# Kernel optimization log

Measured on AMD Instinct MI355X. Metric: run time of the kernel, lower is better.

Reference implementation:

```python
import jax, jax.numpy as jnp
import numpy as np

VOCAB, E, H, HOPS, HEADS = 32000, 128, 256, 3, 4
N, TM, WLEN, TQ = 32, 50, 20, 20


def _gru(x_tbe, h0, Wih, Whh, bih, bhh):
    # x_tbe: [T, B, E] time-major; h0: [B, H]. PyTorch GRU gate order (r, z, n).
    def step(h, xt):
        gi = xt @ Wih.T + bih
        gh = h @ Whh.T + bhh
        ir, iz, inn = jnp.split(gi, 3, axis=-1)
        hr, hz, hn = jnp.split(gh, 3, axis=-1)
        r = jax.nn.sigmoid(ir + hr)
        z = jax.nn.sigmoid(iz + hz)
        n = jnp.tanh(inn + r * hn)
        return (1.0 - z) * n + z * h, None
    h, _ = jax.lax.scan(step, h0, x_tbe)
    return h


def setup_inputs() -> dict:
    key = jax.random.key(0)
    ks = jax.random.split(key, 24)
    f32 = jnp.float32
    emb = jax.random.uniform(ks[0], (VOCAB, E), f32, -3 ** 0.5, 3 ** 0.5)
    emb = emb.at[0].set(0.0)  # padding_idx=0
    s = 0.05
    inp = {
        'stories': jax.random.randint(ks[1], (N, TM, WLEN), 0, VOCAB),
        'questions': jax.random.randint(ks[2], (N, TQ), 0, VOCAB),
        'emb': emb,
        'q_Wih': jax.random.normal(ks[3], (3 * H, E), f32) * s,
        'q_Whh': jax.random.normal(ks[4], (3 * H, H), f32) * s,
        'q_bih': jnp.zeros((3 * H,), f32),
        'q_bhh': jnp.zeros((3 * H,), f32),
        'i_Wih': jax.random.normal(ks[5], (3 * H, E), f32) * s,
        'i_Whh': jax.random.normal(ks[6], (3 * H, H), f32) * s,
        'i_bih': jnp.zeros((3 * H,), f32),
        'i_bhh': jnp.zeros((3 * H,), f32),
        'Wm': jax.random.normal(ks[7], (HOPS, HEADS, H, H), f32) * s,
        'Wo_w': jax.random.normal(ks[8], (HOPS, H, HEADS * H), f32) * s,
        'Wo_b': jnp.full((HOPS, H), 0.01, f32),
        'ft_W1': jax.random.normal(ks[9], (H, H), f32) * s,
        'ft_b1': jnp.full((H,), 0.01, f32),
        'ft_W2': jax.random.normal(ks[10], (H, H), f32) * s,
        'ft_b2': jnp.full((H,), 0.01, f32),
        'g_W1': jax.random.normal(ks[11], (3 * H, 3 * H), f32) * s,
        'g_b1': jnp.full((3 * H,), 0.01, f32),
        'g_W2': jax.random.normal(ks[12], (3 * H, 3 * H), f32) * s,
        'g_b2': jnp.full((3 * H,), 0.01, f32),
        'V_w': jax.random.normal(ks[13], (VOCAB, 3 * H), f32) * s,
    }
    return inp


def reference(stories, questions, emb, q_Wih, q_Whh, q_bih, q_bhh,
              i_Wih, i_Whh, i_bih, i_bhh, Wm, Wo_w, Wo_b,
              ft_W1, ft_b1, ft_W2, ft_b2, g_W1, g_b1, g_W2, g_b2, V_w):
    n, tm, _ = stories.shape
    h = i_Whh.shape[1]
    hops, heads = Wm.shape[0], Wm.shape[1]

    # ---- input module: per-batch-item GRU; hidden state carries across batch items (as in source loop) ----
    story_embs = emb[stories]  # [N, TM, W, E]
    def bstep(hid, se):  # se: [TM, W, E]
        hid2 = _gru(jnp.swapaxes(se, 0, 1), hid, i_Wih, i_Whh, i_bih, i_bhh)
        return hid2, hid2
    _, memory = jax.lax.scan(bstep, jnp.zeros((tm, h), emb.dtype), story_embs)  # [N, TM, H]

    # ---- question module ----
    q_emb = emb[questions]  # [N, TQ, E]
    q = _gru(jnp.swapaxes(q_emb, 0, 1), jnp.zeros((n, h), emb.dtype), q_Wih, q_Whh, q_bih, q_bhh)  # [N, H]

    def ft(x):
        return jax.nn.relu(jax.nn.relu(x @ ft_W1.T + ft_b1) @ ft_W2.T + ft_b2)

    # ---- multi-hop attention controllers ----
    o_k = ft(q)
    buffers = []
    for hp in range(hops):
        proj = jnp.tanh(jnp.einsum('ntd,hed->nhte', memory, Wm[hp]))      # [N,heads,TM,H]
        scores = jax.nn.softmax(jnp.einsum('nhte,ne->nht', proj, o_k), axis=-1)
        rep = jnp.einsum('nht,ntd->nhd', scores, memory)                   # [N,heads,H]
        buf = rep.reshape(n, heads * h) @ Wo_w[hp].T + Wo_b[hp]            # [N,H]
        buffers.append(buf)
        o_k = ft(buf)
    wb = jnp.stack(buffers, axis=1)  # [N, HOPS, H]

    # ---- RM: all-pairs relation MLP (dropout = identity in eval) ----
    npair = hops * hops
    left = jnp.broadcast_to(wb[:, None, :, :], (n, hops, hops, h)).reshape(n, npair, h)
    right = jnp.broadcast_to(wb[:, :, None, :], (n, hops, hops, h)).reshape(n, npair, h)
    qx = jnp.broadcast_to(q[:, None, :], (n, npair, h))
    comb = jnp.concatenate([left, right, qx], axis=-1)                     # [N, HOPS^2, 3H]
    g = jax.nn.relu(jax.nn.relu(comb @ g_W1.T + g_b1) @ g_W2.T + g_b2)
    reasoning = g.sum(axis=1)                                              # [N, 3H]
    return reasoning @ V_w.T                                               # [N, VOCAB]
```

## Files before the change

kernel.cpp:

```cpp
#include <hip/hip_runtime.h>
#include <cmath>

#define VOCABN 32000
#define EE 128
#define HH 256
#define H3 768
#define HOPSN 3
#define HEADSN 4
#define NB 32
#define TMN 50
#define WLENN 20
#define TQN 20
#define NPOS (NB*TMN*WLENN)
#define NQPOS (NB*TQN)

#define OFF_MEM    0
#define OFF_Q      (OFF_MEM + NB*TMN*HH)
#define OFF_OK     (OFF_Q + NB*HH)
#define OFF_WB     (OFF_OK + NB*HH)
#define OFF_REP    (OFF_WB + NB*HOPSN*HH)
#define OFF_REAS   (OFF_REP + NB*HEADSN*HH)
#define OFF_Y1     (OFF_REAS + NB*H3)
#define OFF_PROJ   (OFF_Y1 + NB*9*H3)
#define OFF_GI     (OFF_PROJ + NB*12*TMN*HH)

typedef __fp16 h2 __attribute__((ext_vector_type(2)));

__device__ __forceinline__ float sigm(float x) { return 1.f / (1.f + expf(-x)); }

__device__ __forceinline__ unsigned packh2(float x, float y) {
    h2 h = __builtin_amdgcn_cvt_pkrtz(x, y);
    return __builtin_bit_cast(unsigned, h);
}

__device__ __forceinline__ float fdot2u(unsigned a, unsigned b, float c) {
    return __builtin_amdgcn_fdot2(__builtin_bit_cast(h2, a),
                                  __builtin_bit_cast(h2, b), c, false);
}

#define LW(v, base, i8) { const float4 A_ = reinterpret_cast<const float4*>(base)[2*(i8)];     \
                          const float4 B_ = reinterpret_cast<const float4*>(base)[2*(i8)+1];   \
                          v.x = packh2(A_.x, A_.y); v.y = packh2(A_.z, A_.w);                  \
                          v.z = packh2(B_.x, B_.y); v.w = packh2(B_.z, B_.w); }

#define GIB 64
__global__ __launch_bounds__(768) void k_gi(const int* __restrict__ stories,
                                            const int* __restrict__ questions,
                                            const float* __restrict__ emb,
                                            const float* __restrict__ iWih,
                                            const float* __restrict__ qWih,
                                            const float* __restrict__ ibih, const float* __restrict__ ibhh,
                                            const float* __restrict__ qbih, const float* __restrict__ qbhh,
                                            float* __restrict__ ws)
{
    __shared__ unsigned xs[GIB][EE / 2];
    __fp16* __restrict__ gi = (__fp16*)(ws + OFF_GI);
    const int j = threadIdx.x;
    const bool isq = blockIdx.x >= (NPOS / GIB);
    const int pblk = isq ? (blockIdx.x - NPOS / GIB) : blockIdx.x;
    const int p0 = pblk * GIB;
    const size_t g0 = (isq ? (size_t)NPOS : 0) + (size_t)p0;
    const int* __restrict__ toks = isq ? (questions + p0) : (stories + p0);
    const float* __restrict__ Wih = isq ? qWih : iWih;
    const float* __restrict__ bih = isq ? qbih : ibih;
    const float* __restrict__ bhh = isq ? qbhh : ibhh;
    const float bias = (j < 2 * HH) ? (bih[j] + bhh[j]) : bih[j];
    const float* wrowp = Wih + (size_t)j * EE;
    uint4 v_0, v_1, v_2, v_3, v_4, v_5, v_6, v_7, v_8, v_9, v_10, v_11, v_12, v_13, v_14, v_15;
    LW(v_0, wrowp, 0)  LW(v_1, wrowp, 1)  LW(v_2, wrowp, 2)  LW(v_3, wrowp, 3)
    LW(v_4, wrowp, 4)  LW(v_5, wrowp, 5)  LW(v_6, wrowp, 6)  LW(v_7, wrowp, 7)
    LW(v_8, wrowp, 8)  LW(v_9, wrowp, 9)  LW(v_10, wrowp, 10) LW(v_11, wrowp, 11)
    LW(v_12, wrowp, 12) LW(v_13, wrowp, 13) LW(v_14, wrowp, 14) LW(v_15, wrowp, 15)

    for (int idx = j; idx < GIB * (EE / 2); idx += H3) {
        const int p = idx >> 6, c = idx & 63;
        const int tok = toks[p];
        const float2 e2 = reinterpret_cast<const float2*>(emb + (size_t)tok * EE)[c];
        xs[p][c] = packh2(e2.x, e2.y);
    }
    __syncthreads();

#define DOTG(i) { const uint4 xv = x4[i];                                     \
    acc = fdot2u(xv.x, v_##i.x, acc); acc = fdot2u(xv.y, v_##i.y, acc);       \
    acc = fdot2u(xv.z, v_##i.z, acc); acc = fdot2u(xv.w, v_##i.w, acc); }

    for (int p = 0; p < GIB; ++p) {
        const uint4* x4 = reinterpret_cast<const uint4*>(&xs[p][0]);
        float acc = bias;
        DOTG(0)  DOTG(1)  DOTG(2)  DOTG(3)  DOTG(4)  DOTG(5)  DOTG(6)  DOTG(7)
        DOTG(8)  DOTG(9)  DOTG(10) DOTG(11) DOTG(12) DOTG(13) DOTG(14) DOTG(15)
        gi[(g0 + p) * H3 + j] = (__fp16)acc;
    }
#undef DOTG
}

#define LDSF 22016
__global__ __attribute__((amdgpu_flat_work_group_size(512, 512), amdgpu_waves_per_eu(2, 2)))
void k_gru8(
    const float* __restrict__ iWhh, const float* __restrict__ qWhh,
    const float* __restrict__ ibhh, const float* __restrict__ qbhh,
    float* __restrict__ ws)
{
    __shared__ float ldsb[LDSF];
    unsigned* hp32 = (unsigned*)ldsb;
    float* red = ldsb + 128;
    const int tid = threadIdx.x;
    const int j = tid & 255, kh = tid >> 8;
    const int blk = blockIdx.x;
    const bool isq = blk >= TMN;
    const float* __restrict__ Whh = isq ? qWhh : iWhh;
    const float* row0 = Whh + (size_t)j * HH + kh * 128;
    const float* row1 = Whh + (size_t)(HH + j) * HH + kh * 128;
    const float* row2 = Whh + (size_t)(2 * HH + j) * HH + kh * 128;
    uint4 w0_0, w0_1, w0_2, w0_3, w0_4, w0_5, w0_6, w0_7,
          w0_8, w0_9, w0_10, w0_11, w0_12, w0_13, w0_14, w0_15;
    uint4 w1_0, w1_1, w1_2, w1_3, w1_4, w1_5, w1_6, w1_7,
          w1_8, w1_9, w1_10, w1_11, w1_12, w1_13, w1_14, w1_15;
    uint4 w2_0, w2_1, w2_2, w2_3, w2_4, w2_5, w2_6, w2_7,
          w2_8, w2_9, w2_10, w2_11, w2_12, w2_13, w2_14, w2_15;
    LW(w0_0, row0, 0)  LW(w0_1, row0, 1)  LW(w0_2, row0, 2)  LW(w0_3, row0, 3)
    LW(w0_4, row0, 4)  LW(w0_5, row0, 5)  LW(w0_6, row0, 6)  LW(w0_7, row0, 7)
    LW(w0_8, row0, 8)  LW(w0_9, row0, 9)  LW(w0_10, row0, 10) LW(w0_11, row0, 11)
    LW(w0_12, row0, 12) LW(w0_13, row0, 13) LW(w0_14, row0, 14) LW(w0_15, row0, 15)
    LW(w1_0, row1, 0)  LW(w1_1, row1, 1)  LW(w1_2, row1, 2)  LW(w1_3, row1, 3)
    LW(w1_4, row1, 4)  LW(w1_5, row1, 5)  LW(w1_6, row1, 6)  LW(w1_7, row1, 7)
    LW(w1_8, row1, 8)  LW(w1_9, row1, 9)  LW(w1_10, row1, 10) LW(w1_11, row1, 11)
    LW(w1_12, row1, 12) LW(w1_13, row1, 13) LW(w1_14, row1, 14) LW(w1_15, row1, 15)
    LW(w2_0, row2, 0)  LW(w2_1, row2, 1)  LW(w2_2, row2, 2)  LW(w2_3, row2, 3)
    LW(w2_4, row2, 4)  LW(w2_5, row2, 5)  LW(w2_6, row2, 6)  LW(w2_7, row2, 7)
    LW(w2_8, row2, 8)  LW(w2_9, row2, 9)  LW(w2_10, row2, 10) LW(w2_11, row2, 11)
    LW(w2_12, row2, 12) LW(w2_13, row2, 13) LW(w2_14, row2, 14) LW(w2_15, row2, 15)

    float bnH = 0.f, hstate = 0.f;
    if (kh == 0) bnH = (isq ? qbhh : ibhh)[2 * HH + j];
    if (tid < HH / 2) hp32[tid] = 0u;
    const __fp16* __restrict__ gib = (const __fp16*)(ws + OFF_GI)
                                     + (isq ? (size_t)NPOS * H3 : 0);
    float* __restrict__ memv = ws + OFF_MEM;
    float* __restrict__ qv   = ws + OFF_Q;
    __syncthreads();

#define DOT(i) { const uint4 hv = hp4[kh * 16 + (i)];                        \
    a0 = fdot2u(hv.x, w0_##i.x, a0); a0 = fdot2u(hv.y, w0_##i.y, a0);        \
    a0 = fdot2u(hv.z, w0_##i.z, a0); a0 = fdot2u(hv.w, w0_##i.w, a0);        \
    a1 = fdot2u(hv.x, w1_##i.x, a1); a1 = fdot2u(hv.y, w1_##i.y, a1);        \
    a1 = fdot2u(hv.z, w1_##i.z, a1); a1 = fdot2u(hv.w, w1_##i.w, a1);        \
    a2 = fdot2u(hv.x, w2_##i.x, a2); a2 = fdot2u(hv.y, w2_##i.y, a2);        \
    a2 = fdot2u(hv.z, w2_##i.z, a2); a2 = fdot2u(hv.w, w2_##i.w, a2); }

    const int nOuter = isq ? 1 : NB;
    const int c = isq ? (blk - TMN) : blk;
    for (int n = 0; n < nOuter; ++n) {
        for (int t = 0; t < WLENN; ++t) {
            const int pos = isq ? (c * TQN + t) : ((n * TMN + c) * WLENN + t);
            float gir = 0.f, giz = 0.f, gin = 0.f;
            if (kh == 0) {
                const size_t gb = (size_t)pos * H3;
                gir = (float)gib[gb + j];
                giz = (float)gib[gb + HH + j];
                gin = (float)gib[gb + 2 * HH + j];
            }
            float a0 = 0.f, a1 = 0.f, a2 = 0.f;
            const uint4* hp4 = reinterpret_cast<const uint4*>(hp32);
            DOT(0)  DOT(1)  DOT(2)  DOT(3)  DOT(4)  DOT(5)  DOT(6)  DOT(7)
            DOT(8)  DOT(9)  DOT(10) DOT(11) DOT(12) DOT(13) DOT(14) DOT(15)
            if (kh == 1) { red[j * 5 + 0] = a0; red[j * 5 + 1] = a1; red[j * 5 + 2] = a2; }
            __syncthreads();
            if (kh == 0) {
                const float* rr = red + j * 5;
                const float r  = sigm(a0 + rr[0] + gir);
                const float z  = sigm(a1 + rr[1] + giz);
                const float nn = tanhf(gin + r * (a2 + rr[2] + bnH));
                hstate = (1.f - z) * nn + z * hstate;
                reinterpret_cast<__fp16*>(hp32)[j] = (__fp16)hstate;
                if (t == WLENN - 1) {
                    if (isq) qv[c * HH + j] = hstate;
                    else     memv[(size_t)(n * TMN + c) * HH + j] = hstate;
                }
            }
            __syncthreads();
        }
    }
#undef DOT
}

__global__ __launch_bounds__(256) void k_ft(const float* __restrict__ src, float* __restrict__ dst,
                                            const float* __restrict__ W1, const float* __restrict__ b1,
                                            const float* __restrict__ W2, const float* __restrict__ b2)
{
    __shared__ float xr[HH];
    __shared__ float y1[HH];
    const int n = blockIdx.x, j = threadIdx.x;
    xr[j] = src[n * HH + j];
    __syncthreads();
    float acc = b1[j];
    const float4* w1 = reinterpret_cast<const float4*>(W1 + j * HH);
    #pragma unroll 4
    for (int k4 = 0; k4 < HH / 4; ++k4) {
        const float4 w = w1[k4];
        const float4 x = *reinterpret_cast<const float4*>(&xr[k4 * 4]);
        acc = fmaf(x.x, w.x, fmaf(x.y, w.y, fmaf(x.z, w.z, fmaf(x.w, w.w, acc))));
    }
    y1[j] = fmaxf(acc, 0.f);
    __syncthreads();
    acc = b2[j];
    const float4* w2 = reinterpret_cast<const float4*>(W2 + j * HH);
    #pragma unroll 4
    for (int k4 = 0; k4 < HH / 4; ++k4) {
        const float4 w = w2[k4];
        const float4 x = *reinterpret_cast<const float4*>(&y1[k4 * 4]);
        acc = fmaf(x.x, w.x, fmaf(x.y, w.y, fmaf(x.z, w.z, fmaf(x.w, w.w, acc))));
    }
    dst[n * HH + j] = fmaxf(acc, 0.f);
}

__global__ __launch_bounds__(256) void k_proj(const float* __restrict__ Wm, float* __restrict__ ws)
{
    __shared__ float mem_s[TMN][HH];
    const int n = blockIdx.x / 12, he = blockIdx.x % 12;
    const int e = threadIdx.x;
    const float* __restrict__ memory = ws + OFF_MEM + n * TMN * HH;
    for (int idx = e; idx < TMN * HH; idx += HH)
        (&mem_s[0][0])[idx] = memory[idx];
    __syncthreads();
    float p[TMN];
    #pragma unroll
    for (int t = 0; t < TMN; ++t) p[t] = 0.f;
    const float4* wrow = reinterpret_cast<const float4*>(Wm + ((size_t)he * HH + e) * HH);
    for (int d4 = 0; d4 < HH / 4; ++d4) {
        const float4 w = wrow[d4];
        #pragma unroll
        for (int t = 0; t < TMN; ++t) {
            const float4 m = *reinterpret_cast<const float4*>(&mem_s[t][d4 * 4]);
            p[t] = fmaf(m.x, w.x, fmaf(m.y, w.y, fmaf(m.z, w.z, fmaf(m.w, w.w, p[t]))));
        }
    }
    float* __restrict__ proj = ws + OFF_PROJ + ((size_t)(n * 12 + he) * TMN) * HH;
    #pragma unroll
    for (int t = 0; t < TMN; ++t) proj[t * HH + e] = tanhf(p[t]);
}

__global__ __launch_bounds__(256) void k_attn2(float* __restrict__ ws, int hp)
{
    __shared__ float wred[4][TMN];
    __shared__ float sc[TMN];
    const int n = blockIdx.x / HEADSN, hh = blockIdx.x % HEADSN;
    const int e = threadIdx.x;
    const float* __restrict__ proj = ws + OFF_PROJ + ((size_t)(n * 12 + hp * HEADSN + hh) * TMN) * HH;
    const float* __restrict__ memory = ws + OFF_MEM + n * TMN * HH;
    const float okv = (ws + OFF_OK)[n * HH + e];
    const int lane = e & 63, wv = e >> 6;
    #pragma unroll 10
    for (int t = 0; t < TMN; ++t) {
        float v = proj[t * HH + e] * okv;
        #pragma unroll
        for (int off = 32; off > 0; off >>= 1) v += __shfl_xor(v, off);
        if (lane == 0) wred[wv][t] = v;
    }
    __syncthreads();
    if (e < TMN) sc[e] = wred[0][e] + wred[1][e] + wred[2][e] + wred[3][e];
    __syncthreads();
    if (e == 0) {
        float mx = sc[0];
        for (int t = 1; t < TMN; ++t) mx = fmaxf(mx, sc[t]);
        float sum = 0.f;
        for (int t = 0; t < TMN; ++t) { const float ex = expf(sc[t] - mx); sc[t] = ex; sum += ex; }
        const float inv = 1.f / sum;
        for (int t = 0; t < TMN; ++t) sc[t] *= inv;
    }
    __syncthreads();
    float r = 0.f;
    #pragma unroll 10
    for (int t = 0; t < TMN; ++t) r = fmaf(sc[t], memory[t * HH + e], r);
    (ws + OFF_REP)[(n * HEADSN + hh) * HH + e] = r;
}

__global__ __launch_bounds__(256) void k_buf(const float* __restrict__ Wo_w, const float* __restrict__ Wo_b,
                                             const float* __restrict__ W1, const float* __restrict__ b1,
                                             const float* __restrict__ W2, const float* __restrict__ b2,
                                             float* __restrict__ ws, int hp)
{
    __shared__ float repf[HEADSN * HH];
    __shared__ float bufs[HH];
    __shared__ float y1[HH];
    const int n = blockIdx.x, j = threadIdx.x;
    const float* __restrict__ rep = ws + OFF_REP + n * HEADSN * HH;
    for (int idx = j; idx < HEADSN * HH; idx += HH) repf[idx] = rep[idx];
    __syncthreads();
    float acc = Wo_b[hp * HH + j];
    const float4* wrow = reinterpret_cast<const float4*>(Wo_w + ((size_t)hp * HH + j) * (HEADSN * HH));
    #pragma unroll 4
    for (int c4 = 0; c4 < HEADSN * HH / 4; ++c4) {
        const float4 w = wrow[c4];
        const float4 x = *reinterpret_cast<const float4*>(&repf[c4 * 4]);
        acc = fmaf(x.x, w.x, fmaf(x.y, w.y, fmaf(x.z, w.z, fmaf(x.w, w.w, acc))));
    }
    (ws + OFF_WB)[(n * HOPSN + hp) * HH + j] = acc;
    bufs[j] = acc;
    __syncthreads();
    float a1 = b1[j];
    const float4* w1 = reinterpret_cast<const float4*>(W1 + j * HH);
    #pragma unroll 4
    for (int k4 = 0; k4 < HH / 4; ++k4) {
        const float4 w = w1[k4];
        const float4 x = *reinterpret_cast<const float4*>(&bufs[k4 * 4]);
        a1 = fmaf(x.x, w.x, fmaf(x.y, w.y, fmaf(x.z, w.z, fmaf(x.w, w.w, a1))));
    }
    y1[j] = fmaxf(a1, 0.f);
    __syncthreads();
    float a2 = b2[j];
    const float4* w2 = reinterpret_cast<const float4*>(W2 + j * HH);
    #pragma unroll 4
    for (int k4 = 0; k4 < HH / 4; ++k4) {
        const float4 w = w2[k4];
        const float4 x = *reinterpret_cast<const float4*>(&y1[k4 * 4]);
        a2 = fmaf(x.x, w.x, fmaf(x.y, w.y, fmaf(x.z, w.z, fmaf(x.w, w.w, a2))));
    }
    (ws + OFF_OK)[n * HH + j] = fmaxf(a2, 0.f);
}

__global__ __launch_bounds__(256) void k_rm1(const float* __restrict__ gW1, const float* __restrict__ gb1,
                                             float* __restrict__ ws)
{
    __shared__ float comb[9 * H3];
    const int n = blockIdx.x / 3, ot = blockIdx.x % 3;
    const int o = ot * 256 + threadIdx.x;
    const float* __restrict__ wb = ws + OFF_WB + n * HOPSN * HH;
    const float* __restrict__ qv = ws + OFF_Q + n * HH;
    for (int idx = threadIdx.x; idx < 9 * H3; idx += 256) {
        const int p = idx / H3, cc = idx - p * H3;
        const int ii = p / 3, jj = p % 3;
        float v;
        if (cc < HH)           v = wb[jj * HH + cc];
        else if (cc < 2 * HH)  v = wb[ii * HH + (cc - HH)];
        else                   v = qv[cc - 2 * HH];
        comb[idx] = v;
    }
    __syncthreads();
    float acc[9];
    const float b = gb1[o];
    #pragma unroll
    for (int p = 0; p < 9; ++p) acc[p] = b;
    const float4* w1 = reinterpret_cast<const float4*>(gW1 + (size_t)o * H3);
    for (int c4 = 0; c4 < H3 / 4; ++c4) {
        const float4 w = w1[c4];
        #pragma unroll
        for (int p = 0; p < 9; ++p) {
            const float4 x = *reinterpret_cast<const float4*>(&comb[p * H3 + c4 * 4]);
            acc[p] = fmaf(x.x, w.x, fmaf(x.y, w.y, fmaf(x.z, w.z, fmaf(x.w, w.w, acc[p]))));
        }
    }
    float* __restrict__ y1 = ws + OFF_Y1 + (size_t)n * 9 * H3;
    #pragma unroll
    for (int p = 0; p < 9; ++p) y1[p * H3 + o] = fmaxf(acc[p], 0.f);
}

__global__ __launch_bounds__(256) void k_rm2(const float* __restrict__ gW2, const float* __restrict__ gb2,
                                             float* __restrict__ ws)
{
    __shared__ float y1s[9 * H3];
    const int n = blockIdx.x / 3, ot = blockIdx.x % 3;
    const int o = ot * 256 + threadIdx.x;
    const float* __restrict__ y1 = ws + OFF_Y1 + (size_t)n * 9 * H3;
    for (int idx = threadIdx.x; idx < 9 * H3; idx += 256) y1s[idx] = y1[idx];
    __syncthreads();
    float acc[9];
    const float b = gb2[o];
    #pragma unroll
    for (int p = 0; p < 9; ++p) acc[p] = b;
    const float4* w2 = reinterpret_cast<const float4*>(gW2 + (size_t)o * H3);
    for (int c4 = 0; c4 < H3 / 4; ++c4) {
        const float4 w = w2[c4];
        #pragma unroll
        for (int p = 0; p < 9; ++p) {
            const float4 x = *reinterpret_cast<const float4*>(&y1s[p * H3 + c4 * 4]);
            acc[p] = fmaf(x.x, w.x, fmaf(x.y, w.y, fmaf(x.z, w.z, fmaf(x.w, w.w, acc[p]))));
        }
    }
    float s = 0.f;
    #pragma unroll
    for (int p = 0; p < 9; ++p) s += fmaxf(acc[p], 0.f);
    (ws + OFF_REAS)[n * H3 + o] = s;
}

#define RST 36
__global__ __launch_bounds__(256) void k_out(const float* __restrict__ V_w, const float* __restrict__ ws,
                                             float* __restrict__ out)
{
    __shared__ float rsT[H3 * RST];
    const int tid = threadIdx.x;
    const int v = blockIdx.x * 128 + (tid & 127);
    const int nh = tid >> 7;
    for (int idx = tid; idx < NB * H3; idx += 256) {
        const int n = idx / H3, d = idx - n * H3;
        rsT[d * RST + n] = (ws + OFF_REAS)[idx];
    }
    __syncthreads();
    float acc[16];
    #pragma unroll
    for (int i = 0; i < 16; ++i) acc[i] = 0.f;
    const float4* vw = reinterpret_cast<const float4*>(V_w + (size_t)v * H3);
    for (int d4 = 0; d4 < H3 / 4; ++d4) {
        const float4 w = vw[d4];
        #pragma unroll
        for (int dd = 0; dd < 4; ++dd) {
            const float wd = (dd == 0) ? w.x : (dd == 1) ? w.y : (dd == 2) ? w.z : w.w;
            const float* rr = &rsT[(d4 * 4 + dd) * RST + nh * 16];
            #pragma unroll
            for (int q = 0; q < 4; ++q) {
                const float4 r4 = *reinterpret_cast<const float4*>(rr + 4 * q);
                acc[4 * q + 0] = fmaf(wd, r4.x, acc[4 * q + 0]);
                acc[4 * q + 1] = fmaf(wd, r4.y, acc[4 * q + 1]);
                acc[4 * q + 2] = fmaf(wd, r4.z, acc[4 * q + 2]);
                acc[4 * q + 3] = fmaf(wd, r4.w, acc[4 * q + 3]);
            }
        }
    }
    #pragma unroll
    for (int i = 0; i < 16; ++i)
        out[(size_t)(nh * 16 + i) * VOCABN + v] = acc[i];
}

extern "C" void kernel_launch(void* const* d_in, const int* in_sizes, int n_in,
                              void* d_out, int out_size, void* d_ws, size_t ws_size,
                              hipStream_t stream)
{
    const int*   stories   = (const int*)d_in[0];
    const int*   questions = (const int*)d_in[1];
    const float* emb   = (const float*)d_in[2];
    const float* qWih  = (const float*)d_in[3];
    const float* qWhh  = (const float*)d_in[4];
    const float* qbih  = (const float*)d_in[5];
    const float* qbhh  = (const float*)d_in[6];
    const float* iWih  = (const float*)d_in[7];
    const float* iWhh  = (const float*)d_in[8];
    const float* ibih  = (const float*)d_in[9];
    const float* ibhh  = (const float*)d_in[10];
    const float* Wm    = (const float*)d_in[11];
    const float* Wo_w  = (const float*)d_in[12];
    const float* Wo_b  = (const float*)d_in[13];
    const float* ftW1  = (const float*)d_in[14];
    const float* ftb1  = (const float*)d_in[15];
    const float* ftW2  = (const float*)d_in[16];
    const float* ftb2  = (const float*)d_in[17];
    const float* gW1   = (const float*)d_in[18];
    const float* gb1   = (const float*)d_in[19];
    const float* gW2   = (const float*)d_in[20];
    const float* gb2   = (const float*)d_in[21];
    const float* V_w   = (const float*)d_in[22];
    float* ws  = (float*)d_ws;
    float* out = (float*)d_out;

    hipLaunchKernelGGL(k_gi, dim3((NPOS + NQPOS) / GIB), dim3(H3), 0, stream,
                       stories, questions, emb, iWih, qWih, ibih, ibhh, qbih, qbhh, ws);
    hipLaunchKernelGGL(k_gru8, dim3(TMN + NB), dim3(512), 0, stream,
                       iWhh, qWhh, ibhh, qbhh, ws);
    hipLaunchKernelGGL(k_ft, dim3(NB), dim3(HH), 0, stream, ws + OFF_Q, ws + OFF_OK, ftW1, ftb1, ftW2, ftb2);
    hipLaunchKernelGGL(k_proj, dim3(NB * 12), dim3(256), 0, stream, Wm, ws);
    for (int hp = 0; hp < HOPSN; ++hp) {
        hipLaunchKernelGGL(k_attn2, dim3(NB * HEADSN), dim3(256), 0, stream, ws, hp);
        hipLaunchKernelGGL(k_buf, dim3(NB), dim3(256), 0, stream, Wo_w, Wo_b, ftW1, ftb1, ftW2, ftb2, ws, hp);
    }
    hipLaunchKernelGGL(k_rm1, dim3(NB * 3), dim3(256), 0, stream, gW1, gb1, ws);
    hipLaunchKernelGGL(k_rm2, dim3(NB * 3), dim3(256), 0, stream, gW2, gb2, ws);
    hipLaunchKernelGGL(k_out, dim3(VOCABN / 128), dim3(256), 0, stream, V_w, ws, out);
}
```

Measured before the change: 1.361 ms.

## Fuse feature transform, hop attention, buffer and relation MLP into one tail kernel

Replaces the separate k_ft, per-hop k_attn2/k_buf launches and k_rm1/k_rm2 with one k_tail kernel: one 1024-thread block per batch item keeps memory, o_k, rep and the relation-MLP intermediates in LDS. The goal is to remove about nine kernel launches and the global round-trips of intermediate buffers between them. In exchange, the relation-MLP stage now runs on 32 blocks instead of 96, and each block streams the full g_W1 and g_W2 matrices. The GRU kernel also drops its oversized padded LDS allocation in favour of small exact arrays, which may change how its blocks are placed on CUs.

```diff
diff --git a/kernel.cpp b/kernel.cpp
--- a/kernel.cpp
+++ b/kernel.cpp
@@ -94,16 +94,14 @@
 #undef DOTG
 }
 
-#define LDSF 22016
 __global__ __attribute__((amdgpu_flat_work_group_size(512, 512), amdgpu_waves_per_eu(2, 2)))
-void k_gru8(
+void k_gru7(
     const float* __restrict__ iWhh, const float* __restrict__ qWhh,
     const float* __restrict__ ibhh, const float* __restrict__ qbhh,
     float* __restrict__ ws)
 {
-    __shared__ float ldsb[LDSF];
-    unsigned* hp32 = (unsigned*)ldsb;
-    float* red = ldsb + 128;
+    __shared__ unsigned hp32[HH / 2];
+    __shared__ float red[HH * 5];
     const int tid = threadIdx.x;
     const int j = tid & 255, kh = tid >> 8;
     const int blk = blockIdx.x;
@@ -184,36 +182,6 @@
 #undef DOT
 }
 
-__global__ __launch_bounds__(256) void k_ft(const float* __restrict__ src, float* __restrict__ dst,
-                                            const float* __restrict__ W1, const float* __restrict__ b1,
-                                            const float* __restrict__ W2, const float* __restrict__ b2)
-{
-    __shared__ float xr[HH];
-    __shared__ float y1[HH];
-    const int n = blockIdx.x, j = threadIdx.x;
-    xr[j] = src[n * HH + j];
-    __syncthreads();
-    float acc = b1[j];
-    const float4* w1 = reinterpret_cast<const float4*>(W1 + j * HH);
-    #pragma unroll 4
-    for (int k4 = 0; k4 < HH / 4; ++k4) {
-        const float4 w = w1[k4];
-        const float4 x = *reinterpret_cast<const float4*>(&xr[k4 * 4]);
-        acc = fmaf(x.x, w.x, fmaf(x.y, w.y, fmaf(x.z, w.z, fmaf(x.w, w.w, acc))));
-    }
-    y1[j] = fmaxf(acc, 0.f);
-    __syncthreads();
-    acc = b2[j];
-    const float4* w2 = reinterpret_cast<const float4*>(W2 + j * HH);
-    #pragma unroll 4
-    for (int k4 = 0; k4 < HH / 4; ++k4) {
-        const float4 w = w2[k4];
-        const float4 x = *reinterpret_cast<const float4*>(&y1[k4 * 4]);
-        acc = fmaf(x.x, w.x, fmaf(x.y, w.y, fmaf(x.z, w.z, fmaf(x.w, w.w, acc))));
-    }
-    dst[n * HH + j] = fmaxf(acc, 0.f);
-}
-
 __global__ __launch_bounds__(256) void k_proj(const float* __restrict__ Wm, float* __restrict__ ws)
 {
     __shared__ float mem_s[TMN][HH];
@@ -240,94 +208,115 @@
     for (int t = 0; t < TMN; ++t) proj[t * HH + e] = tanhf(p[t]);
 }
 
-__global__ __launch_bounds__(256) void k_attn2(float* __restrict__ ws, int hp)
-{
-    __shared__ float wred[4][TMN];
-    __shared__ float sc[TMN];
-    const int n = blockIdx.x / HEADSN, hh = blockIdx.x % HEADSN;
-    const int e = threadIdx.x;
-    const float* __restrict__ proj = ws + OFF_PROJ + ((size_t)(n * 12 + hp * HEADSN + hh) * TMN) * HH;
-    const float* __restrict__ memory = ws + OFF_MEM + n * TMN * HH;
-    const float okv = (ws + OFF_OK)[n * HH + e];
-    const int lane = e & 63, wv = e >> 6;
-    #pragma unroll 10
-    for (int t = 0; t < TMN; ++t) {
-        float v = proj[t * HH + e] * okv;
-        #pragma unroll
-        for (int off = 32; off > 0; off >>= 1) v += __shfl_xor(v, off);
-        if (lane == 0) wred[wv][t] = v;
-    }
-    __syncthreads();
-    if (e < TMN) sc[e] = wred[0][e] + wred[1][e] + wred[2][e] + wred[3][e];
-    __syncthreads();
-    if (e == 0) {
-        float mx = sc[0];
-        for (int t = 1; t < TMN; ++t) mx = fmaxf(mx, sc[t]);
-        float sum = 0.f;
-        for (int t = 0; t < TMN; ++t) { const float ex = expf(sc[t] - mx); sc[t] = ex; sum += ex; }
-        const float inv = 1.f / sum;
-        for (int t = 0; t < TMN; ++t) sc[t] *= inv;
-    }
-    __syncthreads();
-    float r = 0.f;
-    #pragma unroll 10
-    for (int t = 0; t < TMN; ++t) r = fmaf(sc[t], memory[t * HH + e], r);
-    (ws + OFF_REP)[(n * HEADSN + hh) * HH + e] = r;
-}
-
-__global__ __launch_bounds__(256) void k_buf(const float* __restrict__ Wo_w, const float* __restrict__ Wo_b,
-                                             const float* __restrict__ W1, const float* __restrict__ b1,
-                                             const float* __restrict__ W2, const float* __restrict__ b2,
-                                             float* __restrict__ ws, int hp)
-{
+__global__ __launch_bounds__(1024) void k_tail(
+    const float* __restrict__ Wo_w, const float* __restrict__ Wo_b,
+    const float* __restrict__ ftW1, const float* __restrict__ ftb1,
+    const float* __restrict__ ftW2, const float* __restrict__ ftb2,
+    const float* __restrict__ gW1, const float* __restrict__ gb1,
+    const float* __restrict__ gW2, const float* __restrict__ gb2,
+    float* __restrict__ ws)
+{
+    __shared__ float mem_s[TMN][HH];
+    __shared__ float ok_s[HH];
+    __shared__ float xr[HH];
+    __shared__ float yft[HH];
+    __shared__ float red4[4][HH];
+    __shared__ float wred[4][4][TMN];
+    __shared__ float sc4[4][TMN];
     __shared__ float repf[HEADSN * HH];
     __shared__ float bufs[HH];
-    __shared__ float y1[HH];
-    const int n = blockIdx.x, j = threadIdx.x;
-    const float* __restrict__ rep = ws + OFF_REP + n * HEADSN * HH;
-    for (int idx = j; idx < HEADSN * HH; idx += HH) repf[idx] = rep[idx];
-    __syncthreads();
-    float acc = Wo_b[hp * HH + j];
-    const float4* wrow = reinterpret_cast<const float4*>(Wo_w + ((size_t)hp * HH + j) * (HEADSN * HH));
-    #pragma unroll 4
-    for (int c4 = 0; c4 < HEADSN * HH / 4; ++c4) {
-        const float4 w = wrow[c4];
-        const float4 x = *reinterpret_cast<const float4*>(&repf[c4 * 4]);
-        acc = fmaf(x.x, w.x, fmaf(x.y, w.y, fmaf(x.z, w.z, fmaf(x.w, w.w, acc))));
-    }
-    (ws + OFF_WB)[(n * HOPSN + hp) * HH + j] = acc;
-    bufs[j] = acc;
-    __syncthreads();
-    float a1 = b1[j];
-    const float4* w1 = reinterpret_cast<const float4*>(W1 + j * HH);
-    #pragma unroll 4
-    for (int k4 = 0; k4 < HH / 4; ++k4) {
-        const float4 w = w1[k4];
-        const float4 x = *reinterpret_cast<const float4*>(&bufs[k4 * 4]);
-        a1 = fmaf(x.x, w.x, fmaf(x.y, w.y, fmaf(x.z, w.z, fmaf(x.w, w.w, a1))));
-    }
-    y1[j] = fmaxf(a1, 0.f);
-    __syncthreads();
-    float a2 = b2[j];
-    const float4* w2 = reinterpret_cast<const float4*>(W2 + j * HH);
-    #pragma unroll 4
-    for (int k4 = 0; k4 < HH / 4; ++k4) {
-        const float4 w = w2[k4];
-        const float4 x = *reinterpret_cast<const float4*>(&y1[k4 * 4]);
-        a2 = fmaf(x.x, w.x, fmaf(x.y, w.y, fmaf(x.z, w.z, fmaf(x.w, w.w, a2))));
-    }
-    (ws + OFF_OK)[n * HH + j] = fmaxf(a2, 0.f);
-}
-
-__global__ __launch_bounds__(256) void k_rm1(const float* __restrict__ gW1, const float* __restrict__ gb1,
-                                             float* __restrict__ ws)
-{
     __shared__ float comb[9 * H3];
-    const int n = blockIdx.x / 3, ot = blockIdx.x % 3;
-    const int o = ot * 256 + threadIdx.x;
+    __shared__ float y1rm[9 * H3];
+    const int n = blockIdx.x;
+    const int tid = threadIdx.x;
+    const int e = tid & 255, hh = tid >> 8;
+    const int lane = tid & 63, wgrp = (tid >> 6) & 3;
+    const float* __restrict__ memory = ws + OFF_MEM + n * TMN * HH;
+    for (int idx = tid; idx < TMN * HH; idx += 1024)
+        (&mem_s[0][0])[idx] = memory[idx];
+    if (tid < HH) xr[tid] = (ws + OFF_Q)[n * HH + tid];
+    __syncthreads();
+
+#define FT_LAYER(WARR, BARR, SRC, DST)                                              \
+    {   float a_ = 0.f;                                                             \
+        const float* wr_ = (WARR) + (size_t)e * HH + hh * 64;                       \
+        const float* sr_ = (SRC) + hh * 64;                                         \
+        _Pragma("unroll")                                                           \
+        for (int k4_ = 0; k4_ < 16; ++k4_) {                                        \
+            const float4 w4_ = *reinterpret_cast<const float4*>(wr_ + 4 * k4_);     \
+            const float4 x4_ = *reinterpret_cast<const float4*>(sr_ + 4 * k4_);     \
+            a_ = fmaf(x4_.x, w4_.x, fmaf(x4_.y, w4_.y,                              \
+                 fmaf(x4_.z, w4_.z, fmaf(x4_.w, w4_.w, a_))));                      \
+        }                                                                           \
+        red4[hh][e] = a_;                                                           \
+        __syncthreads();                                                            \
+        if (tid < HH)                                                               \
+            (DST)[tid] = fmaxf(red4[0][tid] + red4[1][tid] + red4[2][tid]           \
+                               + red4[3][tid] + (BARR)[tid], 0.f);                  \
+        __syncthreads(); }
+
+    FT_LAYER(ftW1, ftb1, xr, yft)
+    FT_LAYER(ftW2, ftb2, yft, ok_s)
+
+    for (int hp = 0; hp < HOPSN; ++hp) {
+        const float* __restrict__ proj =
+            ws + OFF_PROJ + ((size_t)(n * 12 + hp * HEADSN + hh) * TMN) * HH;
+        const float okv = ok_s[e];
+        #pragma unroll 10
+        for (int t = 0; t < TMN; ++t) {
+            float v = proj[t * HH + e] * okv;
+            #pragma unroll
+            for (int off = 32; off > 0; off >>= 1) v += __shfl_xor(v, off);
+            if (lane == 0) wred[hh][wgrp][t] = v;
+        }
+        __syncthreads();
+        if (tid < HEADSN * TMN) {
+            const int h2 = tid / TMN, tt = tid % TMN;
+            sc4[h2][tt] = wred[h2][0][tt] + wred[h2][1][tt] + wred[h2][2][tt] + wred[h2][3][tt];
+        }
+        __syncthreads();
+        if (tid < HEADSN) {
+            float mx = sc4[tid][0];
+            for (int t = 1; t < TMN; ++t) mx = fmaxf(mx, sc4[tid][t]);
+            float sum = 0.f;
+            for (int t = 0; t < TMN; ++t) { const float ex = expf(sc4[tid][t] - mx); sc4[tid][t] = ex; sum += ex; }
+            const float inv = 1.f / sum;
+            for (int t = 0; t < TMN; ++t) sc4[tid][t] *= inv;
+        }
+        __syncthreads();
+        float r = 0.f;
+        #pragma unroll 10
+        for (int t = 0; t < TMN; ++t) r = fmaf(sc4[hh][t], mem_s[t][e], r);
+        repf[hh * HH + e] = r;
+        __syncthreads();
+        float a = 0.f;
+        const float* wrow = Wo_w + ((size_t)hp * HH + e) * (HEADSN * HH) + hh * HH;
+        const float* rp = repf + hh * HH;
+        #pragma unroll 8
+        for (int c4 = 0; c4 < HH / 4; ++c4) {
+            const float4 w4 = *reinterpret_cast<const float4*>(wrow + 4 * c4);
+            const float4 x4 = *reinterpret_cast<const float4*>(rp + 4 * c4);
+            a = fmaf(x4.x, w4.x, fmaf(x4.y, w4.y, fmaf(x4.z, w4.z, fmaf(x4.w, w4.w, a))));
+        }
+        red4[hh][e] = a;
+        __syncthreads();
+        if (tid < HH) {
+            const float b = red4[0][tid] + red4[1][tid] + red4[2][tid] + red4[3][tid]
+                            + Wo_b[hp * HH + tid];
+            bufs[tid] = b;
+            (ws + OFF_WB)[(n * HOPSN + hp) * HH + tid] = b;
+        }
+        __syncthreads();
+        if (hp < HOPSN - 1) {
+            FT_LAYER(ftW1, ftb1, bufs, yft)
+            FT_LAYER(ftW2, ftb2, yft, ok_s)
+        }
+    }
+#undef FT_LAYER
+
     const float* __restrict__ wb = ws + OFF_WB + n * HOPSN * HH;
     const float* __restrict__ qv = ws + OFF_Q + n * HH;
-    for (int idx = threadIdx.x; idx < 9 * H3; idx += 256) {
+    for (int idx = tid; idx < 9 * H3; idx += 1024) {
         const int p = idx / H3, cc = idx - p * H3;
         const int ii = p / 3, jj = p % 3;
         float v;
@@ -337,50 +326,43 @@
         comb[idx] = v;
     }
     __syncthreads();
-    float acc[9];
-    const float b = gb1[o];
-    #pragma unroll
-    for (int p = 0; p < 9; ++p) acc[p] = b;
-    const float4* w1 = reinterpret_cast<const float4*>(gW1 + (size_t)o * H3);
-    for (int c4 = 0; c4 < H3 / 4; ++c4) {
-        const float4 w = w1[c4];
-        #pragma unroll
-        for (int p = 0; p < 9; ++p) {
-            const float4 x = *reinterpret_cast<const float4*>(&comb[p * H3 + c4 * 4]);
-            acc[p] = fmaf(x.x, w.x, fmaf(x.y, w.y, fmaf(x.z, w.z, fmaf(x.w, w.w, acc[p]))));
-        }
-    }
-    float* __restrict__ y1 = ws + OFF_Y1 + (size_t)n * 9 * H3;
-    #pragma unroll
-    for (int p = 0; p < 9; ++p) y1[p * H3 + o] = fmaxf(acc[p], 0.f);
-}
-
-__global__ __launch_bounds__(256) void k_rm2(const float* __restrict__ gW2, const float* __restrict__ gb2,
-                                             float* __restrict__ ws)
-{
-    __shared__ float y1s[9 * H3];
-    const int n = blockIdx.x / 3, ot = blockIdx.x % 3;
-    const int o = ot * 256 + threadIdx.x;
-    const float* __restrict__ y1 = ws + OFF_Y1 + (size_t)n * 9 * H3;
-    for (int idx = threadIdx.x; idx < 9 * H3; idx += 256) y1s[idx] = y1[idx];
-    __syncthreads();
-    float acc[9];
-    const float b = gb2[o];
-    #pragma unroll
-    for (int p = 0; p < 9; ++p) acc[p] = b;
-    const float4* w2 = reinterpret_cast<const float4*>(gW2 + (size_t)o * H3);
-    for (int c4 = 0; c4 < H3 / 4; ++c4) {
-        const float4 w = w2[c4];
-        #pragma unroll
-        for (int p = 0; p < 9; ++p) {
-            const float4 x = *reinterpret_cast<const float4*>(&y1s[p * H3 + c4 * 4]);
-            acc[p] = fmaf(x.x, w.x, fmaf(x.y, w.y, fmaf(x.z, w.z, fmaf(x.w, w.w, acc[p]))));
-        }
-    }
-    float s = 0.f;
-    #pragma unroll
-    for (int p = 0; p < 9; ++p) s += fmaxf(acc[p], 0.f);
-    (ws + OFF_REAS)[n * H3 + o] = s;
+    if (tid < H3) {
+        float acc[9];
+        const float b = gb1[tid];
+        #pragma unroll
+        for (int p = 0; p < 9; ++p) acc[p] = b;
+        const float4* w1 = reinterpret_cast<const float4*>(gW1 + (size_t)tid * H3);
+        for (int c4 = 0; c4 < H3 / 4; ++c4) {
+            const float4 w = w1[c4];
+            #pragma unroll
+            for (int p = 0; p < 9; ++p) {
+                const float4 x = *reinterpret_cast<const float4*>(&comb[p * H3 + c4 * 4]);
+                acc[p] = fmaf(x.x, w.x, fmaf(x.y, w.y, fmaf(x.z, w.z, fmaf(x.w, w.w, acc[p]))));
+            }
+        }
+        #pragma unroll
+        for (int p = 0; p < 9; ++p) y1rm[p * H3 + tid] = fmaxf(acc[p], 0.f);
+    }
+    __syncthreads();
+    if (tid < H3) {
+        float acc[9];
+        const float b = gb2[tid];
+        #pragma unroll
+        for (int p = 0; p < 9; ++p) acc[p] = b;
+        const float4* w2 = reinterpret_cast<const float4*>(gW2 + (size_t)tid * H3);
+        for (int c4 = 0; c4 < H3 / 4; ++c4) {
+            const float4 w = w2[c4];
+            #pragma unroll
+            for (int p = 0; p < 9; ++p) {
+                const float4 x = *reinterpret_cast<const float4*>(&y1rm[p * H3 + c4 * 4]);
+                acc[p] = fmaf(x.x, w.x, fmaf(x.y, w.y, fmaf(x.z, w.z, fmaf(x.w, w.w, acc[p]))));
+            }
+        }
+        float s = 0.f;
+        #pragma unroll
+        for (int p = 0; p < 9; ++p) s += fmaxf(acc[p], 0.f);
+        (ws + OFF_REAS)[n * H3 + tid] = s;
+    }
 }
 
 #define RST 36
@@ -453,15 +435,10 @@
 
     hipLaunchKernelGGL(k_gi, dim3((NPOS + NQPOS) / GIB), dim3(H3), 0, stream,
                        stories, questions, emb, iWih, qWih, ibih, ibhh, qbih, qbhh, ws);
-    hipLaunchKernelGGL(k_gru8, dim3(TMN + NB), dim3(512), 0, stream,
+    hipLaunchKernelGGL(k_gru7, dim3(TMN + NB), dim3(512), 0, stream,
                        iWhh, qWhh, ibhh, qbhh, ws);
-    hipLaunchKernelGGL(k_ft, dim3(NB), dim3(HH), 0, stream, ws + OFF_Q, ws + OFF_OK, ftW1, ftb1, ftW2, ftb2);
     hipLaunchKernelGGL(k_proj, dim3(NB * 12), dim3(256), 0, stream, Wm, ws);
-    for (int hp = 0; hp < HOPSN; ++hp) {
-        hipLaunchKernelGGL(k_attn2, dim3(NB * HEADSN), dim3(256), 0, stream, ws, hp);
-        hipLaunchKernelGGL(k_buf, dim3(NB), dim3(256), 0, stream, Wo_w, Wo_b, ftW1, ftb1, ftW2, ftb2, ws, hp);
-    }
-    hipLaunchKernelGGL(k_rm1, dim3(NB * 3), dim3(256), 0, stream, gW1, gb1, ws);
-    hipLaunchKernelGGL(k_rm2, dim3(NB * 3), dim3(256), 0, stream, gW2, gb2, ws);
+    hipLaunchKernelGGL(k_tail, dim3(NB), dim3(1024), 0, stream,
+                       Wo_w, Wo_b, ftW1, ftb1, ftW2, ftb2, gW1, gb1, gW2, gb2, ws);
     hipLaunchKernelGGL(k_out, dim3(VOCABN / 128), dim3(256), 0, stream, V_w, ws, out);
 }
```

After: 1.374 ms. About the same (+1.0%).
